# Kernel optimization log

Hardware: AMD Instinct MI355X
Metric: run time of the kernel (lower is better)

The kernel has to match this reference:

```python
import jax, jax.numpy as jnp
import numpy as np

# Sizes matching init_kwargs: r=2, J=3 -> K = 1 + (r-1)*J = 4 framelet operators
N, FEAT, K, NNZ = 20000, 64, 4, 320000
NU, GAMMA, J = 2.0, 1.0, 3  # nu, gamma_0 (gamma never updated on this code path)


def setup_inputs() -> dict:
    key = jax.random.key(0)
    ks = jax.random.split(key, 6)
    F = jax.random.normal(ks[0], (N, FEAT), dtype=jnp.float32)
    w_rows = jax.random.randint(ks[1], (K, NNZ), 0, N, dtype=jnp.int32)
    w_cols = jax.random.randint(ks[2], (K, NNZ), 0, N, dtype=jnp.int32)
    # scale ~1/avg_degree so the 14-step fixed-point iteration is contractive/stable
    w_vals = jax.random.normal(ks[3], (K, NNZ), dtype=jnp.float32) / 16.0
    d = jax.random.uniform(ks[4], (N,), dtype=jnp.float32)
    mask = jax.random.uniform(ks[5], (N, 1), dtype=jnp.float32)
    return {"F": F, "w_rows": w_rows, "w_cols": w_cols, "w_vals": w_vals,
            "d": d, "mask": mask, "thres_iter": 15}


def _spmm(rows, cols, vals, X):
    # sparse [N,N] @ dense [N,FEAT] via gather + segment-sum scatter
    return jax.ops.segment_sum(vals[:, None] * X[cols], rows, num_segments=N)


_spmm_shared = jax.vmap(_spmm, in_axes=(0, 0, 0, None))  # K operators, one dense X
_spmm_each = jax.vmap(_spmm, in_axes=(0, 0, 0, 0))       # K operators, K dense Xs


def _soft(x, thr):  # elementwise soft-thresholding: relu(x-t) - relu(-x-t)
    return jax.nn.relu(x - thr) - jax.nn.relu(-x - thr)


def reference(F, w_rows, w_cols, w_vals, d, mask, thres_iter):
    # nu_jl = [0] + [nu / 4^i for i in range(J)]
    nu = jnp.asarray([0.0] + [NU / (4.0 ** i) for i in range(J)], dtype=jnp.float32)  # [K]
    thr = (nu / GAMMA)[:, None, None] * d[None, :, None]  # [K,N,1] per-operator row thresholds
    d1 = d[:, None]                 # [N,1]
    m2 = mask * mask                # [N,1]
    denom = d1 * m2 + GAMMA         # [N,1]
    num_f = d1 * F * m2             # [N,FEAT]
    Y0 = jnp.zeros((K, N, FEAT), dtype=F.dtype)

    def step(carry, _):
        Uk, Y = carry
        # Z(k+1): soft-threshold of W_jl @ Uk + Y_jl / gamma
        Z = _soft(_spmm_shared(w_rows, w_cols, w_vals, Uk) + Y / GAMMA, thr)  # [K,N,FEAT]
        v = Y - GAMMA * Z
        WTV = _spmm_each(w_rows, w_cols, w_vals, v).sum(axis=0)               # [N,FEAT]
        Uk = (num_f - WTV) / denom
        # Y(k+1) dual update
        Y = Y + GAMMA * (_spmm_shared(w_rows, w_cols, w_vals, Uk) - Z)
        return (Uk, Y), None

    n_iter = int(thres_iter) - 1  # while k < thres_iter starting at k=1
    (Uk, _), _ = jax.lax.scan(jax.checkpoint(step), (F, Y0), None, length=n_iter)
    return Uk
```

## Files before the change

kernel.cpp:

```cpp
#include <hip/hip_runtime.h>


constexpr int N_    = 20000;
constexpr int FEAT_ = 64;
constexpr int K_    = 4;
constexpr int NNZ_  = 320000;
constexpr int NF    = N_ * FEAT_;
constexpr int KN    = K_ * N_;
constexpr int NEDGE = K_ * NNZ_;
constexpr int NITER = 14;
constexpr int BLK   = 256;
constexpr int NSB   = (KN + 255) / 256;

constexpr int R_SP  = 10;
constexpr int NB_SP = ((KN + R_SP - 1) / R_SP + 3) / 4;
constexpr int R_WT  = 4;
constexpr int NB_WT = ((N_ + R_WT - 1) / R_WT + 3) / 4;

__constant__ float c_nu[4] = {0.0f, 2.0f, 0.5f, 0.125f};

__device__ __forceinline__ float softf(float x, float t) {
    float a = fabsf(x) - t;
    a = a > 0.0f ? a : 0.0f;
    return copysignf(a, x);
}

__device__ __forceinline__ float bf2f(unsigned short u) {
    union { unsigned int i; float f; } x;
    x.i = ((unsigned int)u) << 16;
    return x.f;
}
__device__ __forceinline__ unsigned short f2bf(float f) {
    union { float f; unsigned int i; } x;
    x.f = f;
    unsigned int r = x.i + 0x7FFFu + ((x.i >> 16) & 1u);
    return (unsigned short)(r >> 16);
}


__global__ __launch_bounds__(BLK) void precompute_kernel(
    const float* __restrict__ F, const float* __restrict__ d,
    const float* __restrict__ mask, float* __restrict__ dm,
    unsigned short* __restrict__ F_bf) {
    int i = blockIdx.x * BLK + threadIdx.x;
    if (i >= NF / 4) return;
    float4 f = ((const float4*)F)[i];
    ushort4 o;
    o.x = f2bf(f.x); o.y = f2bf(f.y); o.z = f2bf(f.z); o.w = f2bf(f.w);
    ((ushort4*)F_bf)[i] = o;
    if ((i & (FEAT_ / 4 - 1)) == 0) {
        int n = i / (FEAT_ / 4);
        dm[n] = d[n] * mask[n] * mask[n];
    }
}

__global__ __launch_bounds__(BLK) void hist_kernel(
    const int* __restrict__ rows, int* __restrict__ cnt) {
    int e = blockIdx.x * BLK + threadIdx.x;
    if (e >= NEDGE) return;
    int k = e / NNZ_;
    atomicAdd(&cnt[rows[e] * K_ + k], 1);
}

__global__ __launch_bounds__(256) void scan1_kernel(
    const int* __restrict__ cnt, int* __restrict__ loc,
    int* __restrict__ bsum) {
    int i = blockIdx.x * 256 + threadIdx.x;
    int x = (i < KN) ? cnt[i] : 0;
    int lane = threadIdx.x & 63, wid = threadIdx.x >> 6;
    int v = x;
    #pragma unroll
    for (int off = 1; off < 64; off <<= 1) {
        int t = __shfl_up(v, off, 64);
        if (lane >= off) v += t;
    }
    __shared__ int ws[4];
    if (lane == 63) ws[wid] = v;
    __syncthreads();
    int add = 0;
    for (int u = 0; u < wid; ++u) add += ws[u];
    v += add;
    if (i < KN) loc[i] = v - x;
    if (threadIdx.x == 255) bsum[blockIdx.x] = v;
}

__global__ __launch_bounds__(512) void scan2_kernel(int* __restrict__ bsum) {
    int tid = threadIdx.x;
    int x = (tid < NSB) ? bsum[tid] : 0;
    int lane = tid & 63, wid = tid >> 6;
    int v = x;
    #pragma unroll
    for (int off = 1; off < 64; off <<= 1) {
        int t = __shfl_up(v, off, 64);
        if (lane >= off) v += t;
    }
    __shared__ int ws[8];
    if (lane == 63) ws[wid] = v;
    __syncthreads();
    int add = 0;
    for (int u = 0; u < wid; ++u) add += ws[u];
    v += add;
    if (tid < NSB) bsum[tid] = v - x;
}

__global__ __launch_bounds__(256) void scan3_kernel(
    const int* __restrict__ loc, const int* __restrict__ bsum,
    int* __restrict__ offs, int* __restrict__ cursor) {
    int i = blockIdx.x * 256 + threadIdx.x;
    if (i < KN) {
        int v = loc[i] + bsum[blockIdx.x];
        offs[i] = v;
        cursor[i] = v;
    }
    if (i == 0) offs[KN] = NEDGE;
}

__global__ __launch_bounds__(BLK) void scatter_kernel(
    const int* __restrict__ rows, const int* __restrict__ cols,
    const float* __restrict__ vals, int* __restrict__ cursor,
    int2* __restrict__ cmeta) {
    int e = blockIdx.x * BLK + threadIdx.x;
    if (e >= NEDGE) return;
    int k = e / NNZ_;
    int pos = atomicAdd(&cursor[rows[e] * K_ + k], 1);
    cmeta[pos] = make_int2(k * N_ + cols[e], __float_as_int(vals[e]));
}


template <int BATCH>
__device__ __forceinline__ void row_accum_bf(
    const int2* __restrict__ cmeta, const ushort4* __restrict__ Xb,
    int beg, int end, int lane, int sub, int q, int padc, float4& acc) {
    for (int ebase = beg; ebase < end; ebase += 64) {
        int n = end - ebase;
        if (n > 64) n = 64;
        int   c_l = padc;
        float v_l = 0.0f;
        if (lane < n) {
            int2 m = cmeta[ebase + lane];
            c_l = m.x;
            v_l = __int_as_float(m.y);
        }
        int iters = (n + 3) >> 2;
        int itersPad = (iters + BATCH - 1) & ~(BATCH - 1);
        for (int it0 = 0; it0 < itersPad; it0 += BATCH) {
            float   vv[BATCH];
            ushort4 xx[BATCH];
            #pragma unroll
            for (int u = 0; u < BATCH; ++u) {
                int j = 4 * (it0 + u) + sub;
                int   c = __shfl(c_l, j, 64);
                vv[u]   = __shfl(v_l, j, 64);
                xx[u]   = Xb[c * (FEAT_ / 4) + q];
            }
            #pragma unroll
            for (int u = 0; u < BATCH; ++u) {
                acc.x += vv[u] * bf2f(xx[u].x);
                acc.y += vv[u] * bf2f(xx[u].y);
                acc.z += vv[u] * bf2f(xx[u].z);
                acc.w += vv[u] * bf2f(xx[u].w);
            }
        }
    }
}

__device__ __forceinline__ void butterfly4(float4& a) {
    #pragma unroll
    for (int m = 16; m <= 32; m <<= 1) {
        a.x += __shfl_xor(a.x, m, 64);
        a.y += __shfl_xor(a.y, m, 64);
        a.z += __shfl_xor(a.z, m, 64);
        a.w += __shfl_xor(a.w, m, 64);
    }
}

template <bool FIRST>
__global__ __launch_bounds__(BLK) void spmm_fused_kernel(
    const int* __restrict__ offs, const int2* __restrict__ cmeta,
    const unsigned short* __restrict__ Xb,
    const float* __restrict__ d, unsigned short* __restrict__ V_bf) {
    int wave = (blockIdx.x * BLK + threadIdx.x) >> 6;
    int lane = threadIdx.x & 63;
    int sub  = lane >> 4, q = lane & 15;
    int base = wave * R_SP;
    if (base >= KN) return;
    int off_l = 0;
    if (lane <= R_SP) {
        int i = base + lane;
        if (i > KN) i = KN;
        off_l = offs[i];
    }
    const ushort4* X4 = (const ushort4*)Xb;
    ushort4* V4 = (ushort4*)V_bf;
    for (int r = 0; r < R_SP; ++r) {
        int w = base + r;
        if (w >= KN) break;
        int k = w & (K_ - 1);
        int n = w >> 2;
        int beg = __shfl(off_l, r, 64);
        int end = __shfl(off_l, r + 1, 64);
        const ushort4* X4m = X4 - (size_t)k * N_ * (FEAT_ / 4);
        float4 acc = {0.f, 0.f, 0.f, 0.f};
        row_accum_bf<4>(cmeta, X4m, beg, end, lane, sub, q, k * N_, acc);
        butterfly4(acc);
        if (sub == 0) {
            int idx4 = (k * N_ + n) * (FEAT_ / 4) + q;
            float thr = c_nu[k] * d[n];
            float4 y;
            if (FIRST) {
                y = make_float4(0.f, 0.f, 0.f, 0.f);
            } else {
                ushort4 vp = V4[idx4];
                y.x = acc.x + bf2f(vp.x); y.y = acc.y + bf2f(vp.y);
                y.z = acc.z + bf2f(vp.z); y.w = acc.w + bf2f(vp.w);
            }
            ushort4 o;
            o.x = f2bf(y.x - softf(acc.x + y.x, thr));
            o.y = f2bf(y.y - softf(acc.y + y.y, thr));
            o.z = f2bf(y.z - softf(acc.z + y.z, thr));
            o.w = f2bf(y.w - softf(acc.w + y.w, thr));
            V4[idx4] = o;
        }
    }
}

__global__ __launch_bounds__(BLK) void wtv_u_kernel(
    const int* __restrict__ offs, const int2* __restrict__ cmeta,
    const unsigned short* __restrict__ V_bf,
    const float* __restrict__ F, const float* __restrict__ dm,
    float* __restrict__ U, unsigned short* __restrict__ U_bf) {
    int wave = (blockIdx.x * BLK + threadIdx.x) >> 6;
    int lane = threadIdx.x & 63;
    int sub  = lane >> 4, q = lane & 15;
    int base = wave * R_WT;
    if (base >= N_) return;
    int off_l = 0;
    if (lane <= K_ * R_WT) {
        int i = K_ * base + lane;
        if (i > KN) i = KN;
        off_l = offs[i];
    }
    const ushort4* V4 = (const ushort4*)V_bf;
    for (int r = 0; r < R_WT; ++r) {
        int n = base + r;
        if (n >= N_) break;
        int beg = __shfl(off_l, K_ * r, 64);
        int end = __shfl(off_l, K_ * r + K_, 64);
        float4 acc = {0.f, 0.f, 0.f, 0.f};
        row_accum_bf<8>(cmeta, V4, beg, end, lane, sub, q, 0, acc);
        butterfly4(acc);
        if (sub == 0) {
            int idx4 = n * (FEAT_ / 4) + q;
            float dmv = dm[n];
            float r2 = 1.0f / (dmv + 1.0f);
            float4 f = ((const float4*)F)[idx4];
            float4 o;
            o.x = (dmv * f.x - acc.x) * r2; o.y = (dmv * f.y - acc.y) * r2;
            o.z = (dmv * f.z - acc.z) * r2; o.w = (dmv * f.w - acc.w) * r2;
            ((float4*)U)[idx4] = o;
            ushort4 ob;
            ob.x = f2bf(o.x); ob.y = f2bf(o.y);
            ob.z = f2bf(o.z); ob.w = f2bf(o.w);
            ((ushort4*)U_bf)[idx4] = ob;
        }
    }
}

extern "C" void kernel_launch(void* const* d_in, const int* in_sizes, int n_in,
                              void* d_out, int out_size, void* d_ws, size_t ws_size,
                              hipStream_t stream) {
    const float* F      = (const float*)d_in[0];
    const int*   w_rows = (const int*)d_in[1];
    const int*   w_cols = (const int*)d_in[2];
    const float* w_vals = (const float*)d_in[3];
    const float* d      = (const float*)d_in[4];
    const float* mask   = (const float*)d_in[5];
    float* U = (float*)d_out;

    int2* cmeta          = (int2*)d_ws;
    unsigned short* V_bf = (unsigned short*)(cmeta + NEDGE);
    unsigned short* U_bf = V_bf + (size_t)KN * FEAT_;
    unsigned short* F_bf = U_bf + NF;
    float* dm     = (float*)(F_bf + NF);
    int*   cnt    = (int*)(dm + N_);
    int*   loc    = cnt + KN;
    int*   bsum   = loc + KN;
    int*   offs   = bsum + 512;
    int*   cursor = offs + KN + 1;

    const int gEdge = NEDGE / BLK;
    const int gNF4  = (NF / 4) / BLK;

    hipMemsetAsync(cnt, 0, (size_t)KN * 4, stream);
    precompute_kernel<<<gNF4, BLK, 0, stream>>>(F, d, mask, dm, F_bf);
    hist_kernel<<<gEdge, BLK, 0, stream>>>(w_rows, cnt);
    scan1_kernel<<<NSB, 256, 0, stream>>>(cnt, loc, bsum);
    scan2_kernel<<<1, 512, 0, stream>>>(bsum);
    scan3_kernel<<<NSB, 256, 0, stream>>>(loc, bsum, offs, cursor);
    scatter_kernel<<<gEdge, BLK, 0, stream>>>(w_rows, w_cols, w_vals,
                                              cursor, cmeta);

    spmm_fused_kernel<true><<<NB_SP, BLK, 0, stream>>>(offs, cmeta, F_bf, d, V_bf);
    for (int it = 0; it < NITER; ++it) {
        wtv_u_kernel<<<NB_WT, BLK, 0, stream>>>(offs, cmeta, V_bf,
                                                F, dm, U, U_bf);
        if (it < NITER - 1)
            spmm_fused_kernel<false><<<NB_SP, BLK, 0, stream>>>(offs, cmeta,
                                                                U_bf, d, V_bf);
    }
}
```

Baseline: 967.5 us.

## Privatize histogram counters and interleave per-operator segments in WTV gather

The histogram kernel now spreads its atomics over eight private copies of the count array, chosen by block index, and scan1 sums the copies. This is meant to reduce atomic contention. The WTV kernel now keeps one accumulator per row for its four rows and loops over operators k on the outside. Each (row, k) segment goes through row_accum_bf with unroll 4, which gives more independent gathers in flight per wave. In exchange the memset and scan read more data, and each call walks shorter segments, which may raise loop overhead and register pressure.

```diff
diff --git a/kernel.cpp b/kernel.cpp
--- a/kernel.cpp
+++ b/kernel.cpp
@@ -11,6 +11,7 @@
 constexpr int NITER = 14;
 constexpr int BLK   = 256;
 constexpr int NSB   = (KN + 255) / 256;
+constexpr int NCPY  = 8;
 
 constexpr int R_SP  = 10;
 constexpr int NB_SP = ((KN + R_SP - 1) / R_SP + 3) / 4;
@@ -55,18 +56,23 @@
 }
 
 __global__ __launch_bounds__(BLK) void hist_kernel(
-    const int* __restrict__ rows, int* __restrict__ cnt) {
+    const int* __restrict__ rows, int* __restrict__ cnt8) {
     int e = blockIdx.x * BLK + threadIdx.x;
     if (e >= NEDGE) return;
     int k = e / NNZ_;
-    atomicAdd(&cnt[rows[e] * K_ + k], 1);
+    int copy = blockIdx.x & (NCPY - 1);
+    atomicAdd(&cnt8[copy * KN + rows[e] * K_ + k], 1);
 }
 
 __global__ __launch_bounds__(256) void scan1_kernel(
-    const int* __restrict__ cnt, int* __restrict__ loc,
+    const int* __restrict__ cnt8, int* __restrict__ loc,
     int* __restrict__ bsum) {
     int i = blockIdx.x * 256 + threadIdx.x;
-    int x = (i < KN) ? cnt[i] : 0;
+    int x = 0;
+    if (i < KN) {
+        #pragma unroll
+        for (int c = 0; c < NCPY; ++c) x += cnt8[c * KN + i];
+    }
     int lane = threadIdx.x & 63, wid = threadIdx.x >> 6;
     int v = x;
     #pragma unroll
@@ -241,22 +247,32 @@
         off_l = offs[i];
     }
     const ushort4* V4 = (const ushort4*)V_bf;
+    float4 acc[R_WT];
+    #pragma unroll
+    for (int r = 0; r < R_WT; ++r) acc[r] = make_float4(0.f, 0.f, 0.f, 0.f);
+    for (int kk = 0; kk < K_; ++kk) {
+        #pragma unroll
+        for (int r = 0; r < R_WT; ++r) {
+            int n = base + r;
+            if (n >= N_) break;
+            int beg = __shfl(off_l, K_ * r + kk, 64);
+            int end = __shfl(off_l, K_ * r + kk + 1, 64);
+            row_accum_bf<4>(cmeta, V4, beg, end, lane, sub, q, 0, acc[r]);
+        }
+    }
+    #pragma unroll
     for (int r = 0; r < R_WT; ++r) {
         int n = base + r;
         if (n >= N_) break;
-        int beg = __shfl(off_l, K_ * r, 64);
-        int end = __shfl(off_l, K_ * r + K_, 64);
-        float4 acc = {0.f, 0.f, 0.f, 0.f};
-        row_accum_bf<8>(cmeta, V4, beg, end, lane, sub, q, 0, acc);
-        butterfly4(acc);
+        butterfly4(acc[r]);
         if (sub == 0) {
             int idx4 = n * (FEAT_ / 4) + q;
             float dmv = dm[n];
             float r2 = 1.0f / (dmv + 1.0f);
             float4 f = ((const float4*)F)[idx4];
             float4 o;
-            o.x = (dmv * f.x - acc.x) * r2; o.y = (dmv * f.y - acc.y) * r2;
-            o.z = (dmv * f.z - acc.z) * r2; o.w = (dmv * f.w - acc.w) * r2;
+            o.x = (dmv * f.x - acc[r].x) * r2; o.y = (dmv * f.y - acc[r].y) * r2;
+            o.z = (dmv * f.z - acc[r].z) * r2; o.w = (dmv * f.w - acc[r].w) * r2;
             ((float4*)U)[idx4] = o;
             ushort4 ob;
             ob.x = f2bf(o.x); ob.y = f2bf(o.y);
@@ -282,8 +298,8 @@
     unsigned short* U_bf = V_bf + (size_t)KN * FEAT_;
     unsigned short* F_bf = U_bf + NF;
     float* dm     = (float*)(F_bf + NF);
-    int*   cnt    = (int*)(dm + N_);
-    int*   loc    = cnt + KN;
+    int*   cnt8   = (int*)(dm + N_);
+    int*   loc    = cnt8 + NCPY * KN;
     int*   bsum   = loc + KN;
     int*   offs   = bsum + 512;
     int*   cursor = offs + KN + 1;
@@ -291,10 +307,10 @@
     const int gEdge = NEDGE / BLK;
     const int gNF4  = (NF / 4) / BLK;
 
-    hipMemsetAsync(cnt, 0, (size_t)KN * 4, stream);
+    hipMemsetAsync(cnt8, 0, (size_t)NCPY * KN * 4, stream);
     precompute_kernel<<<gNF4, BLK, 0, stream>>>(F, d, mask, dm, F_bf);
-    hist_kernel<<<gEdge, BLK, 0, stream>>>(w_rows, cnt);
-    scan1_kernel<<<NSB, 256, 0, stream>>>(cnt, loc, bsum);
+    hist_kernel<<<gEdge, BLK, 0, stream>>>(w_rows, cnt8);
+    scan1_kernel<<<NSB, 256, 0, stream>>>(cnt8, loc, bsum);
     scan2_kernel<<<1, 512, 0, stream>>>(bsum);
     scan3_kernel<<<NSB, 256, 0, stream>>>(loc, bsum, offs, cursor);
     scatter_kernel<<<gEdge, BLK, 0, stream>>>(w_rows, w_cols, w_vals,
```

Result: slower. 1.003 ms (+3.7%).
